# Kernel tuning notes

Measured on AMD Instinct MI355X. Metric: run time of the kernel, lower is better.

## Reference

```python
import jax, jax.numpy as jnp
import numpy as np

CLIP = 10.0  # tanh clipping constant (Kool et al. C=10)


def setup_inputs() -> dict:
    key = jax.random.key(0)
    kq, kk, kv, km = jax.random.split(key, 4)
    B, M, N, D = 16, 2048, 2048, 128
    Q = jax.random.normal(kq, (B, M, D), dtype=jnp.float32)
    K = jax.random.normal(kk, (B, N, D), dtype=jnp.float32)
    V = jax.random.normal(kv, (B, N, D), dtype=jnp.float32)
    # mask: [B, N, 1] bool; True means "forbidden" (set logit to -inf).
    # p=0.3 so every row keeps plenty of valid keys (no all-masked rows).
    mask = jax.random.bernoulli(km, 0.3, (B, N, 1))
    return {"Q": Q, "K": K, "V": V, "mask": mask}


def reference(Q, K, V, mask):
    d_k = jnp.asarray(K.shape[-1], dtype=Q.dtype)
    # logits: [B, M, N]
    logits = jnp.einsum("bmd,bnd->bmn", Q, K) / jnp.sqrt(d_k)
    logits = CLIP * jnp.tanh(logits)
    # mask [B, N, 1] -> [B, 1, N], broadcast over query dim
    mask_t = jnp.transpose(mask, (0, 2, 1))
    logits = jnp.where(mask_t, -jnp.inf, logits)
    probs = jax.nn.softmax(logits, axis=-1)
    return jnp.einsum("bmn,bnd->bmd", probs, V)
```

## Files before the change

### kernel.cpp

```cpp
#include <hip/hip_runtime.h>
#include <hip/hip_fp16.h>

typedef _Float16 h8 __attribute__((ext_vector_type(8)));
typedef _Float16 h4 __attribute__((ext_vector_type(4)));
typedef float f32x4 __attribute__((ext_vector_type(4)));
typedef float f32x16 __attribute__((ext_vector_type(16)));
typedef unsigned int u32x2 __attribute__((ext_vector_type(2)));
typedef unsigned int u32x4 __attribute__((ext_vector_type(4)));

#define MFMA16(a, b, c) __builtin_amdgcn_mfma_f32_16x16x32_f16((a), (b), (c), 0, 0, 0)
#define MFMA32(a, b, c) __builtin_amdgcn_mfma_f32_32x32x16_f16((a), (b), (c), 0, 0, 0)

static constexpr int MM = 2048, NN = 2048, DD = 128;
static constexpr int KT = 64, NT = NN / KT;
static constexpr size_t KV_IMG = (size_t)16 * 32 * 16384;
static constexpr size_t WS_NEED = 2 * KV_IMG + 4096 + 32768 * 4;

static constexpr float C1 = 0.25503487f;
static constexpr float C2 = 28.853900817779268f;
static constexpr float CVALID = 14.426950408889634f;
static constexpr float CMASK = -1.0e30f;

__device__ inline void glds16(const void* g, void* l) {
  __builtin_amdgcn_global_load_lds(
      (const __attribute__((address_space(1))) void*)g,
      (__attribute__((address_space(3))) void*)l, 16, 0, 0);
}

__global__ __launch_bounds__(256) void prep_bias(const void* __restrict__ mraw,
                                                 float* __restrict__ biasC) {
  const int tid = threadIdx.x;
  const unsigned int* mw = (const unsigned int*)mraw;
  const unsigned char* mby = (const unsigned char*)mraw;
  int okW = 1;
  for (int w = tid; w < 8192; w += 256) {
    unsigned int v = mw[w];
    okW &= (v == 0u || v == 1u || v == 0x3f800000u) ? 1 : 0;
  }
  __shared__ int sW;
  if (tid == 0) sW = 1;
  __syncthreads();
  if (!okW) atomicAnd(&sW, 0);
  __syncthreads();
  const int i = blockIdx.x * 256 + tid;
  bool masked = sW ? (mw[i] != 0u) : (mby[i] != 0);
  biasC[i] = masked ? CMASK : CVALID;
}

__global__ __launch_bounds__(256) void prep_all(
    const float* __restrict__ K, const float* __restrict__ V,
    const void* __restrict__ mraw, unsigned char* __restrict__ kimg,
    unsigned char* __restrict__ vimg, unsigned long long* __restrict__ m64) {
  const int id = blockIdx.x;
  const int tid = threadIdx.x;
  if (id >= 1024) {
    const unsigned int* mw = (const unsigned int*)mraw;
    const unsigned char* mby = (const unsigned char*)mraw;
    int okW = 1;
    for (int w = tid; w < 8192; w += 256) {
      unsigned int v = mw[w];
      okW &= (v == 0u || v == 1u || v == 0x3f800000u) ? 1 : 0;
    }
    __shared__ int sW;
    if (tid == 0) sW = 1;
    __syncthreads();
    if (!okW) atomicAnd(&sW, 0);
    __syncthreads();
    const int p = (id - 1024) * 256 + tid;
    const int base = p * 64;
    unsigned long long bits = 0ull;
    if (sW) {
#pragma unroll 8
      for (int k = 0; k < 64; ++k)
        bits |= (unsigned long long)(mw[base + k] != 0u ? 1 : 0) << k;
    } else {
#pragma unroll 8
      for (int k = 0; k < 64; ++k)
        bits |= (unsigned long long)(mby[base + k] != 0 ? 1 : 0) << k;
    }
    m64[p] = bits;
    return;
  }
  const int bt = id & 511;
  if (id < 512) {
    const float* src = K + (size_t)bt * KT * DD;
    unsigned char* dst = kimg + (size_t)bt * 16384;
#pragma unroll
    for (int it = 0; it < 4; ++it) {
      const int key = (tid >> 4) + 16 * it;
      const int o = tid & 15;
      f32x4 a = *(const f32x4*)(src + key * DD + 8 * o);
      f32x4 c = *(const f32x4*)(src + key * DD + 8 * o + 4);
      h8 hv;
#pragma unroll
      for (int j = 0; j < 4; ++j) {
        hv[j] = (_Float16)a[j];
        hv[j + 4] = (_Float16)c[j];
      }
      *(h8*)(dst + key * 256 + ((16 * o) ^ ((key & 7) << 4))) = hv;
    }
  } else {
    const float* src = V + (size_t)bt * KT * DD;
    unsigned char* dst = vimg + (size_t)bt * 16384;
    const int d = tid & 127;
    const int half = tid >> 7;
#pragma unroll
    for (int ki = 0; ki < 4; ++ki) {
      const int koct = half * 4 + ki;
      h8 w;
#pragma unroll
      for (int q = 0; q < 8; ++q)
        w[q] = (_Float16)src[(8 * koct + q) * DD + d];
      *(h8*)(dst + d * 128 + 16 * (koct ^ (d & 7))) = w;
    }
  }
}

__global__ __launch_bounds__(512, 2) void attn_main(
    const float* __restrict__ Qg, const unsigned char* __restrict__ kimg,
    const unsigned char* __restrict__ vimg,
    const unsigned long long* __restrict__ mask64, float* __restrict__ out) {
  __shared__ __align__(16) unsigned char smem[68096];
  const int tid = threadIdx.x;
  const int lane = tid & 63;
  const int wv = tid >> 6;
  const int l31 = lane & 31;
  const int hp = lane >> 5;
  const int qg = wv >> 1;
  const int h = wv & 1;
  const int bid = blockIdx.x;
  const int b = 2 * (bid & 7) + (bid >> 7);
  const int mt = (bid >> 3) & 15;
  const int m0 = mt * 128 + qg * 32;

  h8 qa[8];
  {
    const float* qr = Qg + ((size_t)b * MM + m0 + l31) * DD;
#pragma unroll
    for (int st = 0; st < 8; ++st) {
      const int d0 = 16 * st + 8 * hp;
      f32x4 a = *(const f32x4*)(qr + d0);
      f32x4 c = *(const f32x4*)(qr + d0 + 4);
      h8 hi;
#pragma unroll
      for (int j = 0; j < 4; ++j) {
        hi[j] = (_Float16)a[j];
        hi[j + 4] = (_Float16)c[j];
      }
      qa[st] = hi;
    }
  }

  f32x16 oacc[4];
#pragma unroll
  for (int dc = 0; dc < 4; ++dc)
#pragma unroll
    for (int j = 0; j < 16; ++j) oacc[dc][j] = 0.f;
  float rsl = 0.f;

  const unsigned char* kib = kimg + (size_t)b * 32 * 16384;
  const unsigned char* vib = vimg + (size_t)b * 32 * 16384;
  const unsigned long long* mtile = mask64 + (size_t)b * 32;

#pragma unroll
  for (int i = 0; i < 2; ++i) {
    const int off = wv * 2048 + i * 1024;
    glds16(kib + off + lane * 16, smem + off);
    glds16(vib + off + lane * 16, smem + 16384 + off);
  }
  __syncthreads();

  const int kr = 32 * h + l31;
  const int krow = kr << 8;
  const int ksw = (kr & 7) << 4;
  const int baseSh = 32 * h + 4 * hp;

  for (int tn = 0; tn < NT; ++tn) {
    const unsigned char* kbuf = smem + (tn & 1) * 32768;
    const unsigned char* vbuf = kbuf + 16384;
    if (tn + 1 < NT) {
      unsigned char* nbuf = smem + ((tn + 1) & 1) * 32768;
      const unsigned char* ks = kib + (size_t)(tn + 1) * 16384;
      const unsigned char* vs = vib + (size_t)(tn + 1) * 16384;
#pragma unroll
      for (int i = 0; i < 2; ++i) {
        const int off = wv * 2048 + i * 1024;
        glds16(ks + off + lane * 16, nbuf + off);
        glds16(vs + off + lane * 16, nbuf + 16384 + off);
      }
    }
    const unsigned long long mbits = mtile[tn];

    f32x16 s;
#pragma unroll
    for (int j = 0; j < 16; ++j) s[j] = 0.f;
    __builtin_amdgcn_s_setprio(1);
#pragma unroll
    for (int st = 0; st < 8; ++st) {
      h8 kf = *(const h8*)(kbuf + krow + ((32 * st + 16 * hp) ^ ksw));
      s = MFMA32(kf, qa[st], s);
    }
    __builtin_amdgcn_s_setprio(0);

    float p[16];
#pragma unroll
    for (int q = 0; q < 4; ++q) {
      const unsigned nib = (unsigned)(mbits >> (baseSh + 8 * q)) & 0xFu;
#pragma unroll
      for (int i = 0; i < 4; ++i) {
        const int rg = 4 * q + i;
        const float Cc = ((nib >> i) & 1u) ? CMASK : CVALID;
        const float u = __builtin_amdgcn_exp2f(s[rg] * C1);
        const float pv = __builtin_amdgcn_exp2f(
            fmaf(-C2, __builtin_amdgcn_rcpf(u + 1.0f), Cc));
        p[rg] = pv;
        rsl += pv;
      }
    }
    unsigned pkA[4], pkB[4];
#pragma unroll
    for (int q = 0; q < 4; ++q) {
      pkA[q] = __builtin_bit_cast(
          unsigned, __builtin_amdgcn_cvt_pkrtz(p[4 * q + 0], p[4 * q + 1]));
      pkB[q] = __builtin_bit_cast(
          unsigned, __builtin_amdgcn_cvt_pkrtz(p[4 * q + 2], p[4 * q + 3]));
    }
    h8 pb[2];
#pragma unroll
    for (int ks = 0; ks < 2; ++ks) {
      u32x2 sa = __builtin_amdgcn_permlane32_swap(pkA[2 * ks], pkA[2 * ks + 1],
                                                  false, false);
      u32x2 sb = __builtin_amdgcn_permlane32_swap(pkB[2 * ks], pkB[2 * ks + 1],
                                                  false, false);
      u32x4 w = {sa[0], sb[0], sa[1], sb[1]};
      pb[ks] = __builtin_bit_cast(h8, w);
    }
    __builtin_amdgcn_s_setprio(1);
#pragma unroll
    for (int dc = 0; dc < 4; ++dc) {
      const int d = 32 * dc + l31;
      const int vrow = d << 7;
      const int vsw = (d & 7) << 4;
      h8 vf0 = *(const h8*)(vbuf + vrow + ((64 * h + 16 * hp) ^ vsw));
      h8 vf1 = *(const h8*)(vbuf + vrow + ((64 * h + 32 + 16 * hp) ^ vsw));
      oacc[dc] = MFMA32(vf0, pb[0], oacc[dc]);
      oacc[dc] = MFMA32(vf1, pb[1], oacc[dc]);
    }
    __builtin_amdgcn_s_setprio(0);
    __syncthreads();
  }

  u32x2 rr = __builtin_amdgcn_permlane32_swap(__float_as_uint(rsl),
                                              __float_as_uint(rsl), false,
                                              false);
  const float totH = __uint_as_float(rr[0]) + __uint_as_float(rr[1]);

  float* olds = (float*)smem;
  float* rs1 = (float*)(smem + 67584);
  const int row = qg * 32 + l31;
  if (h == 1) {
#pragma unroll
    for (int dc = 0; dc < 4; ++dc)
#pragma unroll
      for (int q = 0; q < 4; ++q) {
        f32x4 v = {oacc[dc][4 * q + 0], oacc[dc][4 * q + 1],
                   oacc[dc][4 * q + 2], oacc[dc][4 * q + 3]};
        *(f32x4*)&olds[row * 132 + 32 * dc + 8 * q + 4 * hp] = v;
      }
    if (hp == 0) rs1[row] = totH;
  }
  __syncthreads();
  if (h == 0) {
    const float inv = __builtin_amdgcn_rcpf(totH + rs1[row]);
#pragma unroll
    for (int dc = 0; dc < 4; ++dc)
#pragma unroll
      for (int q = 0; q < 4; ++q) {
        float* pp = &olds[row * 132 + 32 * dc + 8 * q + 4 * hp];
        f32x4 v = *(const f32x4*)pp;
        v[0] = (v[0] + oacc[dc][4 * q + 0]) * inv;
        v[1] = (v[1] + oacc[dc][4 * q + 1]) * inv;
        v[2] = (v[2] + oacc[dc][4 * q + 2]) * inv;
        v[3] = (v[3] + oacc[dc][4 * q + 3]) * inv;
        *(f32x4*)pp = v;
      }
  }
  __syncthreads();
  float* ob = out + ((size_t)b * MM + mt * 128) * DD;
#pragma unroll
  for (int c = 0; c < 8; ++c) {
    const int idx = c * 2048 + tid * 4;
    const int r2 = idx >> 7, col = idx & 127;
    *(f32x4*)&ob[r2 * 128 + col] = *(const f32x4*)&olds[r2 * 132 + col];
  }
}

__global__ __launch_bounds__(256, 2) void attn_fallback(
    const float* __restrict__ Qg, const float* __restrict__ Kg,
    const float* __restrict__ Vg, const float* __restrict__ biasC,
    float* __restrict__ out) {
  __shared__ __align__(16) unsigned char smem[51456];
  const int tid = threadIdx.x;
  const int lane = tid & 63;
  const int wv = tid >> 6;
  const int r = lane & 15;
  const int g = lane >> 4;
  const int rw = wv >> 1;
  const int h = wv & 1;
  const int b = blockIdx.x >> 5;
  const int mt = blockIdx.x & 31;
  const int m0 = mt * 64 + rw * 32;

  float* blds = (float*)(smem + 43264);
  {
    const float* cb = biasC + b * NN;
#pragma unroll
    for (int i = 0; i < 8; ++i) blds[tid + 256 * i] = cb[tid + 256 * i];
  }
  h8 qh[2][4];
  {
    const float* qb = Qg + ((size_t)b * MM + m0) * DD;
#pragma unroll
    for (int rf = 0; rf < 2; ++rf) {
      const float* qr = qb + (16 * rf + r) * DD;
#pragma unroll
      for (int t = 0; t < 4; ++t) {
        f32x4 a = *(const f32x4*)(qr + 32 * t + 8 * g);
        f32x4 c = *(const f32x4*)(qr + 32 * t + 8 * g + 4);
        h8 hi;
#pragma unroll
        for (int j = 0; j < 4; ++j) {
          hi[j] = (_Float16)a[j];
          hi[j + 4] = (_Float16)c[j];
        }
        qh[rf][t] = hi;
      }
    }
  }
  f32x4 acc[2][8];
#pragma unroll
  for (int rf = 0; rf < 2; ++rf)
#pragma unroll
    for (int cd = 0; cd < 8; ++cd) acc[rf][cd] = (f32x4){0.f, 0.f, 0.f, 0.f};
  float rs[2][4] = {{0.f, 0.f, 0.f, 0.f}, {0.f, 0.f, 0.f, 0.f}};
  const float* kb = Kg + (size_t)b * NN * DD;
  const float* vbp = Vg + (size_t)b * NN * DD;
  _Float16* plds = (_Float16*)(smem + 32768 + wv * 2560);
  const int bk0 = tid >> 5, bd0 = tid & 31;
  const int bk1 = (256 + tid) >> 5, bd1 = tid & 31;
  f32x4 kpre[8], vpre[8];
#pragma unroll
  for (int i = 0; i < 8; ++i) kpre[i] = *(const f32x4*)(kb + i * 1024 + tid * 4);
#pragma unroll
  for (int q = 0; q < 4; ++q) {
    vpre[q] = *(const f32x4*)(vbp + (4 * bk0 + q) * DD + 4 * bd0);
    vpre[4 + q] = *(const f32x4*)(vbp + (4 * bk1 + q) * DD + 4 * bd1);
  }
  for (int tn = 0; tn < NT; ++tn) {
#pragma unroll
    for (int i = 0; i < 8; ++i) {
      const int flat = i * 1024 + tid * 4;
      const int kkey = flat >> 7;
      const int d0 = flat & 127;
      h4 hv;
#pragma unroll
      for (int j = 0; j < 4; ++j) hv[j] = (_Float16)kpre[i][j];
      *(h4*)(smem + (kkey << 8) + ((d0 << 1) ^ ((kkey & 7) << 4))) = hv;
    }
#pragma unroll
    for (int it = 0; it < 2; ++it) {
      const int bk = it ? bk1 : bk0;
      const int bd = it ? bd1 : bd0;
#pragma unroll
      for (int p = 0; p < 4; ++p) {
        h4 w;
#pragma unroll
        for (int q = 0; q < 4; ++q) w[q] = (_Float16)vpre[it * 4 + q][p];
        const int d = 4 * bd + p;
        *(h4*)(smem + 16384 + (d << 7) +
               ((bk << 3) ^ (((d >> 1) & 7) << 4))) = w;
      }
    }
    if (tn + 1 < NT) {
      const float* ks = kb + (tn + 1) * KT * DD;
      const float* vs = vbp + (tn + 1) * KT * DD;
#pragma unroll
      for (int i = 0; i < 8; ++i) kpre[i] = *(const f32x4*)(ks + i * 1024 + tid * 4);
#pragma unroll
      for (int q = 0; q < 4; ++q) {
        vpre[q] = *(const f32x4*)(vs + (4 * bk0 + q) * DD + 4 * bd0);
        vpre[4 + q] = *(const f32x4*)(vs + (4 * bk1 + q) * DD + 4 * bd1);
      }
    }
    __syncthreads();
#pragma unroll
    for (int c = 0; c < 2; ++c) {
      f32x4 S0 = {0.f, 0.f, 0.f, 0.f}, S1 = {0.f, 0.f, 0.f, 0.f};
      const int kkey = h * 32 + 16 * c + r;
      const int krow = kkey << 8;
      const int ksw = (kkey & 7) << 4;
#pragma unroll
      for (int t = 0; t < 4; ++t) {
        h8 kf = *(const h8*)(smem + krow + ((64 * t + 16 * g) ^ ksw));
        S0 = MFMA16(qh[0][t], kf, S0);
        S1 = MFMA16(qh[1][t], kf, S1);
      }
      const float Cc = blds[tn * KT + kkey];
#pragma unroll
      for (int j = 0; j < 4; ++j) {
        float u0 = __builtin_amdgcn_exp2f(S0[j] * C1);
        float p0 = __builtin_amdgcn_exp2f(
            fmaf(-C2, __builtin_amdgcn_rcpf(u0 + 1.0f), Cc));
        rs[0][j] += p0;
        plds[(4 * g + j) * 40 + 16 * c + r] = (_Float16)p0;
        float u1 = __builtin_amdgcn_exp2f(S1[j] * C1);
        float p1 = __builtin_amdgcn_exp2f(
            fmaf(-C2, __builtin_amdgcn_rcpf(u1 + 1.0f), Cc));
        rs[1][j] += p1;
        plds[(16 + 4 * g + j) * 40 + 16 * c + r] = (_Float16)p1;
      }
    }
    h8 a0 = *(const h8*)((unsigned char*)plds + r * 80 + 16 * g);
    h8 a1 = *(const h8*)((unsigned char*)plds + (16 + r) * 80 + 16 * g);
#pragma unroll
    for (int cd = 0; cd < 8; ++cd) {
      const int d = 16 * cd + r;
      h8 vf = *(const h8*)(smem + 16384 + (d << 7) +
                           ((64 * h + 16 * g) ^ (((d >> 1) & 7) << 4)));
      acc[0][cd] = MFMA16(a0, vf, acc[0][cd]);
      acc[1][cd] = MFMA16(a1, vf, acc[1][cd]);
    }
    __syncthreads();
  }
#pragma unroll
  for (int rf = 0; rf < 2; ++rf)
#pragma unroll
    for (int j = 0; j < 4; ++j) {
      float v = rs[rf][j];
      v += __shfl_xor(v, 1);
      v += __shfl_xor(v, 2);
      v += __shfl_xor(v, 4);
      v += __shfl_xor(v, 8);
      rs[rf][j] = v;
    }
  float* olds = (float*)smem;
  float* rslds = (float*)(smem + 43008);
  if (h == 1) {
    float* my = olds + rw * 4096;
#pragma unroll
    for (int rf = 0; rf < 2; ++rf)
#pragma unroll
      for (int cd = 0; cd < 8; ++cd)
#pragma unroll
        for (int j = 0; j < 4; ++j)
          my[(16 * rf + 4 * g + j) * 128 + 16 * cd + r] = acc[rf][cd][j];
    if (r == 0) {
#pragma unroll
      for (int rf = 0; rf < 2; ++rf)
#pragma unroll
        for (int j = 0; j < 4; ++j)
          rslds[rw * 32 + 16 * rf + 4 * g + j] = rs[rf][j];
    }
  }
  __syncthreads();
  if (h == 0) {
    const float* ot = olds + rw * 4096;
    float* ob = out + ((size_t)b * MM + m0) * DD;
#pragma unroll
    for (int rf = 0; rf < 2; ++rf)
#pragma unroll
      for (int j = 0; j < 4; ++j) {
        const int rl = 16 * rf + 4 * g + j;
        const float tot = rs[rf][j] + rslds[rw * 32 + rl];
        const float inv = __builtin_amdgcn_rcpf(tot);
#pragma unroll
        for (int cd = 0; cd < 8; ++cd) {
          float v = acc[rf][cd][j] + ot[rl * 128 + 16 * cd + r];
          ob[rl * DD + 16 * cd + r] = v * inv;
        }
      }
  }
}

extern "C" void kernel_launch(void* const* d_in, const int* in_sizes, int n_in,
                              void* d_out, int out_size, void* d_ws, size_t ws_size,
                              hipStream_t stream) {
  const float* Q = (const float*)d_in[0];
  const float* K = (const float*)d_in[1];
  const float* V = (const float*)d_in[2];
  const void* mask = d_in[3];
  float* out = (float*)d_out;
  if (ws_size >= WS_NEED) {
    unsigned char* kimg = (unsigned char*)d_ws;
    unsigned char* vimg = kimg + KV_IMG;
    unsigned long long* m64 = (unsigned long long*)(vimg + KV_IMG);
    prep_all<<<dim3(1026), dim3(256), 0, stream>>>(K, V, mask, kimg, vimg, m64);
    attn_main<<<dim3(256), dim3(512), 0, stream>>>(Q, kimg, vimg, m64, out);
  } else {
    float* biasC = (float*)d_ws;
    prep_bias<<<dim3(128), dim3(256), 0, stream>>>(mask, biasC);
    attn_fallback<<<dim3(512), dim3(256), 0, stream>>>(Q, K, V, biasC, out);
  }
}
```

Before: 82.02 us.

## Fold mask into V and row-sum MFMA, enlarge key tile to 128

Masking moves out of the softmax loop. Masked V rows are zeroed during preprocessing, and the row sum is computed by an MFMA against a per-key fp16 indicator vector, so the per-element mask select and scalar accumulation go away. The K image is pre-scaled by C1 to drop a multiply per logit. The key tile doubles to 128 with larger double-buffered LDS (about 135KB), which lowers occupancy to one block per CU in exchange for fewer barriers per key. Mask preprocessing becomes its own kernel launch, adding a dependency ahead of prep_kv.

Result: faster. 75.18 us (-8.3%).

```diff
diff --git a/kernel.cpp b/kernel.cpp
--- a/kernel.cpp
+++ b/kernel.cpp
@@ -12,9 +12,10 @@
 #define MFMA32(a, b, c) __builtin_amdgcn_mfma_f32_32x32x16_f16((a), (b), (c), 0, 0, 0)
 
 static constexpr int MM = 2048, NN = 2048, DD = 128;
-static constexpr int KT = 64, NT = NN / KT;
-static constexpr size_t KV_IMG = (size_t)16 * 32 * 16384;
-static constexpr size_t WS_NEED = 2 * KV_IMG + 4096 + 32768 * 4;
+static constexpr int KT = 128, NT = NN / KT;
+static constexpr size_t KV_IMG = (size_t)16 * 16 * 32768;
+static constexpr size_t IND_IMG = 65536;
+static constexpr size_t WS_NEED = 2 * KV_IMG + IND_IMG + 32768 * 4;
 
 static constexpr float C1 = 0.25503487f;
 static constexpr float C2 = 28.853900817779268f;
@@ -25,6 +26,26 @@
   __builtin_amdgcn_global_load_lds(
       (const __attribute__((address_space(1))) void*)g,
       (__attribute__((address_space(3))) void*)l, 16, 0, 0);
+}
+
+__global__ __launch_bounds__(256) void prep_mask(const void* __restrict__ mraw,
+                                                 _Float16* __restrict__ ind) {
+  const int tid = threadIdx.x;
+  const unsigned int* mw = (const unsigned int*)mraw;
+  const unsigned char* mby = (const unsigned char*)mraw;
+  int okW = 1;
+  for (int w = tid; w < 8192; w += 256) {
+    unsigned int v = mw[w];
+    okW &= (v == 0u || v == 1u || v == 0x3f800000u) ? 1 : 0;
+  }
+  __shared__ int sW;
+  if (tid == 0) sW = 1;
+  __syncthreads();
+  if (!okW) atomicAnd(&sW, 0);
+  __syncthreads();
+  const int i = blockIdx.x * 256 + tid;
+  bool masked = sW ? (mw[i] != 0u) : (mby[i] != 0);
+  ind[i] = masked ? (_Float16)0.0f : (_Float16)1.0f;
 }
 
 __global__ __launch_bounds__(256) void prep_bias(const void* __restrict__ mraw,
@@ -47,44 +68,17 @@
   biasC[i] = masked ? CMASK : CVALID;
 }
 
-__global__ __launch_bounds__(256) void prep_all(
-    const float* __restrict__ K, const float* __restrict__ V,
-    const void* __restrict__ mraw, unsigned char* __restrict__ kimg,
-    unsigned char* __restrict__ vimg, unsigned long long* __restrict__ m64) {
+__global__ __launch_bounds__(256) void prep_kv(const float* __restrict__ K,
+                                               const float* __restrict__ V,
+                                               const _Float16* __restrict__ ind,
+                                               unsigned char* __restrict__ kimg,
+                                               unsigned char* __restrict__ vimg) {
   const int id = blockIdx.x;
   const int tid = threadIdx.x;
-  if (id >= 1024) {
-    const unsigned int* mw = (const unsigned int*)mraw;
-    const unsigned char* mby = (const unsigned char*)mraw;
-    int okW = 1;
-    for (int w = tid; w < 8192; w += 256) {
-      unsigned int v = mw[w];
-      okW &= (v == 0u || v == 1u || v == 0x3f800000u) ? 1 : 0;
-    }
-    __shared__ int sW;
-    if (tid == 0) sW = 1;
-    __syncthreads();
-    if (!okW) atomicAnd(&sW, 0);
-    __syncthreads();
-    const int p = (id - 1024) * 256 + tid;
-    const int base = p * 64;
-    unsigned long long bits = 0ull;
-    if (sW) {
-#pragma unroll 8
-      for (int k = 0; k < 64; ++k)
-        bits |= (unsigned long long)(mw[base + k] != 0u ? 1 : 0) << k;
-    } else {
-#pragma unroll 8
-      for (int k = 0; k < 64; ++k)
-        bits |= (unsigned long long)(mby[base + k] != 0 ? 1 : 0) << k;
-    }
-    m64[p] = bits;
-    return;
-  }
-  const int bt = id & 511;
+  const int bt = (id < 512) ? id : (id - 512);
   if (id < 512) {
-    const float* src = K + (size_t)bt * KT * DD;
-    unsigned char* dst = kimg + (size_t)bt * 16384;
+    const float* src = K + (size_t)bt * 64 * DD;
+    unsigned char* dst = kimg + (size_t)(bt >> 1) * 32768 + (bt & 1) * 16384;
 #pragma unroll
     for (int it = 0; it < 4; ++it) {
       const int key = (tid >> 4) + 16 * it;
@@ -94,14 +88,15 @@
       h8 hv;
 #pragma unroll
       for (int j = 0; j < 4; ++j) {
-        hv[j] = (_Float16)a[j];
-        hv[j + 4] = (_Float16)c[j];
+        hv[j] = (_Float16)(a[j] * C1);
+        hv[j + 4] = (_Float16)(c[j] * C1);
       }
       *(h8*)(dst + key * 256 + ((16 * o) ^ ((key & 7) << 4))) = hv;
     }
   } else {
-    const float* src = V + (size_t)bt * KT * DD;
-    unsigned char* dst = vimg + (size_t)bt * 16384;
+    const float* src = V + (size_t)bt * 64 * DD;
+    unsigned char* dst = vimg + (size_t)(bt >> 1) * 32768;
+    const _Float16* ip = ind + (size_t)bt * 64;
     const int d = tid & 127;
     const int half = tid >> 7;
 #pragma unroll
@@ -110,17 +105,18 @@
       h8 w;
 #pragma unroll
       for (int q = 0; q < 8; ++q)
-        w[q] = (_Float16)src[(8 * koct + q) * DD + d];
-      *(h8*)(dst + d * 128 + 16 * (koct ^ (d & 7))) = w;
-    }
-  }
-}
-
-__global__ __launch_bounds__(512, 2) void attn_main(
+        w[q] = (_Float16)src[(8 * koct + q) * DD + d] * ip[8 * koct + q];
+      const int g = (bt & 1) * 8 + koct;
+      *(h8*)(dst + d * 256 + ((g * 16) ^ ((d & 7) << 4))) = w;
+    }
+  }
+}
+
+__global__ __launch_bounds__(512, 1) void attn_main(
     const float* __restrict__ Qg, const unsigned char* __restrict__ kimg,
-    const unsigned char* __restrict__ vimg,
-    const unsigned long long* __restrict__ mask64, float* __restrict__ out) {
-  __shared__ __align__(16) unsigned char smem[68096];
+    const unsigned char* __restrict__ vimg, const _Float16* __restrict__ indg,
+    float* __restrict__ out) {
+  __shared__ __align__(16) unsigned char smem[135680];
   const int tid = threadIdx.x;
   const int lane = tid & 63;
   const int wv = tid >> 6;
@@ -156,116 +152,121 @@
   for (int dc = 0; dc < 4; ++dc)
 #pragma unroll
     for (int j = 0; j < 16; ++j) oacc[dc][j] = 0.f;
-  float rsl = 0.f;
-
-  const unsigned char* kib = kimg + (size_t)b * 32 * 16384;
-  const unsigned char* vib = vimg + (size_t)b * 32 * 16384;
-  const unsigned long long* mtile = mask64 + (size_t)b * 32;
-
-#pragma unroll
-  for (int i = 0; i < 2; ++i) {
-    const int off = wv * 2048 + i * 1024;
+  f32x16 rsacc;
+#pragma unroll
+  for (int j = 0; j < 16; ++j) rsacc[j] = 0.f;
+
+  const unsigned char* kib = kimg + (size_t)b * 16 * 32768;
+  const unsigned char* vib = vimg + (size_t)b * 16 * 32768;
+  unsigned char* sind = smem + 131072;
+
+#pragma unroll
+  for (int i = 0; i < 4; ++i) {
+    const int off = wv * 4096 + i * 1024;
     glds16(kib + off + lane * 16, smem + off);
-    glds16(vib + off + lane * 16, smem + 16384 + off);
-  }
-  __syncthreads();
-
-  const int kr = 32 * h + l31;
-  const int krow = kr << 8;
-  const int ksw = (kr & 7) << 4;
-  const int baseSh = 32 * h + 4 * hp;
+    glds16(vib + off + lane * 16, smem + 32768 + off);
+  }
+  if (wv < 4)
+    glds16((const unsigned char*)indg + (size_t)b * 4096 + wv * 1024 + lane * 16,
+           sind + wv * 1024);
+  __syncthreads();
+
+  const int ksw = (l31 & 7) << 4;
 
   for (int tn = 0; tn < NT; ++tn) {
-    const unsigned char* kbuf = smem + (tn & 1) * 32768;
-    const unsigned char* vbuf = kbuf + 16384;
+    const unsigned char* kbuf = smem + (tn & 1) * 65536;
+    const unsigned char* vbuf = kbuf + 32768;
     if (tn + 1 < NT) {
-      unsigned char* nbuf = smem + ((tn + 1) & 1) * 32768;
-      const unsigned char* ks = kib + (size_t)(tn + 1) * 16384;
-      const unsigned char* vs = vib + (size_t)(tn + 1) * 16384;
-#pragma unroll
-      for (int i = 0; i < 2; ++i) {
-        const int off = wv * 2048 + i * 1024;
+      unsigned char* nbuf = smem + ((tn + 1) & 1) * 65536;
+      const unsigned char* ks = kib + (size_t)(tn + 1) * 32768;
+      const unsigned char* vs = vib + (size_t)(tn + 1) * 32768;
+#pragma unroll
+      for (int i = 0; i < 4; ++i) {
+        const int off = wv * 4096 + i * 1024;
         glds16(ks + off + lane * 16, nbuf + off);
-        glds16(vs + off + lane * 16, nbuf + 16384 + off);
-      }
-    }
-    const unsigned long long mbits = mtile[tn];
-
-    f32x16 s;
-#pragma unroll
-    for (int j = 0; j < 16; ++j) s[j] = 0.f;
-    __builtin_amdgcn_s_setprio(1);
-#pragma unroll
-    for (int st = 0; st < 8; ++st) {
-      h8 kf = *(const h8*)(kbuf + krow + ((32 * st + 16 * hp) ^ ksw));
-      s = MFMA32(kf, qa[st], s);
-    }
-    __builtin_amdgcn_s_setprio(0);
-
-    float p[16];
-#pragma unroll
-    for (int q = 0; q < 4; ++q) {
-      const unsigned nib = (unsigned)(mbits >> (baseSh + 8 * q)) & 0xFu;
-#pragma unroll
-      for (int i = 0; i < 4; ++i) {
-        const int rg = 4 * q + i;
-        const float Cc = ((nib >> i) & 1u) ? CMASK : CVALID;
-        const float u = __builtin_amdgcn_exp2f(s[rg] * C1);
-        const float pv = __builtin_amdgcn_exp2f(
-            fmaf(-C2, __builtin_amdgcn_rcpf(u + 1.0f), Cc));
-        p[rg] = pv;
-        rsl += pv;
-      }
-    }
-    unsigned pkA[4], pkB[4];
-#pragma unroll
-    for (int q = 0; q < 4; ++q) {
-      pkA[q] = __builtin_bit_cast(
-          unsigned, __builtin_amdgcn_cvt_pkrtz(p[4 * q + 0], p[4 * q + 1]));
-      pkB[q] = __builtin_bit_cast(
-          unsigned, __builtin_amdgcn_cvt_pkrtz(p[4 * q + 2], p[4 * q + 3]));
-    }
-    h8 pb[2];
-#pragma unroll
-    for (int ks = 0; ks < 2; ++ks) {
-      u32x2 sa = __builtin_amdgcn_permlane32_swap(pkA[2 * ks], pkA[2 * ks + 1],
-                                                  false, false);
-      u32x2 sb = __builtin_amdgcn_permlane32_swap(pkB[2 * ks], pkB[2 * ks + 1],
-                                                  false, false);
-      u32x4 w = {sa[0], sb[0], sa[1], sb[1]};
-      pb[ks] = __builtin_bit_cast(h8, w);
-    }
-    __builtin_amdgcn_s_setprio(1);
-#pragma unroll
-    for (int dc = 0; dc < 4; ++dc) {
-      const int d = 32 * dc + l31;
-      const int vrow = d << 7;
-      const int vsw = (d & 7) << 4;
-      h8 vf0 = *(const h8*)(vbuf + vrow + ((64 * h + 16 * hp) ^ vsw));
-      h8 vf1 = *(const h8*)(vbuf + vrow + ((64 * h + 32 + 16 * hp) ^ vsw));
-      oacc[dc] = MFMA32(vf0, pb[0], oacc[dc]);
-      oacc[dc] = MFMA32(vf1, pb[1], oacc[dc]);
-    }
-    __builtin_amdgcn_s_setprio(0);
+        glds16(vs + off + lane * 16, nbuf + 32768 + off);
+      }
+    }
+
+#pragma unroll
+    for (int c = 0; c < 2; ++c) {
+      f32x16 s;
+#pragma unroll
+      for (int j = 0; j < 16; ++j) s[j] = 0.f;
+      const int krow = (64 * h + 32 * c + l31) << 8;
+      __builtin_amdgcn_s_setprio(1);
+#pragma unroll
+      for (int st = 0; st < 8; ++st) {
+        h8 kf = *(const h8*)(kbuf + krow + ((32 * st + 16 * hp) ^ ksw));
+        s = MFMA32(kf, qa[st], s);
+      }
+      __builtin_amdgcn_s_setprio(0);
+
+      unsigned pkA[4], pkB[4];
+#pragma unroll
+      for (int jq = 0; jq < 4; ++jq) {
+        float p[4];
+#pragma unroll
+        for (int i = 0; i < 4; ++i) {
+          const float u = __builtin_amdgcn_exp2f(s[4 * jq + i]);
+          p[i] = __builtin_amdgcn_exp2f(
+              fmaf(-C2, __builtin_amdgcn_rcpf(u + 1.0f), CVALID));
+        }
+        pkA[jq] = __builtin_bit_cast(unsigned,
+                                     __builtin_amdgcn_cvt_pkrtz(p[0], p[1]));
+        pkB[jq] = __builtin_bit_cast(unsigned,
+                                     __builtin_amdgcn_cvt_pkrtz(p[2], p[3]));
+      }
+      h8 pb[2];
+#pragma unroll
+      for (int ks = 0; ks < 2; ++ks) {
+        u32x2 sa = __builtin_amdgcn_permlane32_swap(pkA[2 * ks],
+                                                    pkA[2 * ks + 1], false,
+                                                    false);
+        u32x2 sb = __builtin_amdgcn_permlane32_swap(pkB[2 * ks],
+                                                    pkB[2 * ks + 1], false,
+                                                    false);
+        u32x4 w = {sa[0], sb[0], sa[1], sb[1]};
+        pb[ks] = __builtin_bit_cast(h8, w);
+      }
+
+      __builtin_amdgcn_s_setprio(1);
+#pragma unroll
+      for (int ks = 0; ks < 2; ++ks) {
+        const int gks = 2 * c + ks;
+        h8 ia = *(const h8*)(sind + tn * 256 + 128 * h + 32 * gks + 16 * hp);
+        rsacc = MFMA32(ia, pb[ks], rsacc);
+      }
+#pragma unroll
+      for (int dc = 0; dc < 4; ++dc) {
+        const int vrow = (32 * dc + l31) << 8;
+#pragma unroll
+        for (int ks = 0; ks < 2; ++ks) {
+          const int gks = 2 * c + ks;
+          h8 vf = *(const h8*)(vbuf + vrow +
+                               ((128 * h + 32 * gks + 16 * hp) ^ ksw));
+          oacc[dc] = MFMA32(vf, pb[ks], oacc[dc]);
+        }
+      }
+      __builtin_amdgcn_s_setprio(0);
+    }
     __syncthreads();
   }
 
-  u32x2 rr = __builtin_amdgcn_permlane32_swap(__float_as_uint(rsl),
-                                              __float_as_uint(rsl), false,
-                                              false);
-  const float totH = __uint_as_float(rr[0]) + __uint_as_float(rr[1]);
-
-  float* olds = (float*)smem;
-  float* rs1 = (float*)(smem + 67584);
+  const float totH = rsacc[0];
+
+  float* rs1 = (float*)(smem + 135168);
+  unsigned char* olds = smem;
   const int row = qg * 32 + l31;
   if (h == 1) {
 #pragma unroll
     for (int dc = 0; dc < 4; ++dc)
 #pragma unroll
-      for (int q = 0; q < 4; ++q) {
-        f32x4 v = {oacc[dc][4 * q + 0], oacc[dc][4 * q + 1],
-                   oacc[dc][4 * q + 2], oacc[dc][4 * q + 3]};
-        *(f32x4*)&olds[row * 132 + 32 * dc + 8 * q + 4 * hp] = v;
+      for (int jq = 0; jq < 4; ++jq) {
+        f32x4 v = {oacc[dc][4 * jq + 0], oacc[dc][4 * jq + 1],
+                   oacc[dc][4 * jq + 2], oacc[dc][4 * jq + 3]};
+        const int dbyte = (32 * dc + 8 * jq + 4 * hp) * 4;
+        *(f32x4*)(olds + row * 512 + (dbyte ^ ((row & 31) << 4))) = v;
       }
     if (hp == 0) rs1[row] = totH;
   }
@@ -275,23 +276,26 @@
 #pragma unroll
     for (int dc = 0; dc < 4; ++dc)
 #pragma unroll
-      for (int q = 0; q < 4; ++q) {
-        float* pp = &olds[row * 132 + 32 * dc + 8 * q + 4 * hp];
+      for (int jq = 0; jq < 4; ++jq) {
+        const int dbyte = (32 * dc + 8 * jq + 4 * hp) * 4;
+        float* pp = (float*)(olds + row * 512 + (dbyte ^ ((row & 31) << 4)));
         f32x4 v = *(const f32x4*)pp;
-        v[0] = (v[0] + oacc[dc][4 * q + 0]) * inv;
-        v[1] = (v[1] + oacc[dc][4 * q + 1]) * inv;
-        v[2] = (v[2] + oacc[dc][4 * q + 2]) * inv;
-        v[3] = (v[3] + oacc[dc][4 * q + 3]) * inv;
+        v[0] = (v[0] + oacc[dc][4 * jq + 0]) * inv;
+        v[1] = (v[1] + oacc[dc][4 * jq + 1]) * inv;
+        v[2] = (v[2] + oacc[dc][4 * jq + 2]) * inv;
+        v[3] = (v[3] + oacc[dc][4 * jq + 3]) * inv;
         *(f32x4*)pp = v;
       }
   }
   __syncthreads();
   float* ob = out + ((size_t)b * MM + mt * 128) * DD;
 #pragma unroll
-  for (int c = 0; c < 8; ++c) {
-    const int idx = c * 2048 + tid * 4;
-    const int r2 = idx >> 7, col = idx & 127;
-    *(f32x4*)&ob[r2 * 128 + col] = *(const f32x4*)&olds[r2 * 132 + col];
+  for (int it = 0; it < 8; ++it) {
+    const int byte = it * 8192 + tid * 16;
+    const int r2 = byte >> 9;
+    const int g16 = byte & 511;
+    *(f32x4*)((unsigned char*)ob + byte) =
+        *(const f32x4*)(olds + r2 * 512 + (g16 ^ ((r2 & 31) << 4)));
   }
 }
 
@@ -356,7 +360,7 @@
     vpre[q] = *(const f32x4*)(vbp + (4 * bk0 + q) * DD + 4 * bd0);
     vpre[4 + q] = *(const f32x4*)(vbp + (4 * bk1 + q) * DD + 4 * bd1);
   }
-  for (int tn = 0; tn < NT; ++tn) {
+  for (int tn = 0; tn < 32; ++tn) {
 #pragma unroll
     for (int i = 0; i < 8; ++i) {
       const int flat = i * 1024 + tid * 4;
@@ -381,9 +385,9 @@
                ((bk << 3) ^ (((d >> 1) & 7) << 4))) = w;
       }
     }
-    if (tn + 1 < NT) {
-      const float* ks = kb + (tn + 1) * KT * DD;
-      const float* vs = vbp + (tn + 1) * KT * DD;
+    if (tn + 1 < 32) {
+      const float* ks = kb + (tn + 1) * 64 * DD;
+      const float* vs = vbp + (tn + 1) * 64 * DD;
 #pragma unroll
       for (int i = 0; i < 8; ++i) kpre[i] = *(const f32x4*)(ks + i * 1024 + tid * 4);
 #pragma unroll
@@ -405,7 +409,7 @@
         S0 = MFMA16(qh[0][t], kf, S0);
         S1 = MFMA16(qh[1][t], kf, S1);
       }
-      const float Cc = blds[tn * KT + kkey];
+      const float Cc = blds[tn * 64 + kkey];
 #pragma unroll
       for (int j = 0; j < 4; ++j) {
         float u0 = __builtin_amdgcn_exp2f(S0[j] * C1);
@@ -493,9 +497,10 @@
   if (ws_size >= WS_NEED) {
     unsigned char* kimg = (unsigned char*)d_ws;
     unsigned char* vimg = kimg + KV_IMG;
-    unsigned long long* m64 = (unsigned long long*)(vimg + KV_IMG);
-    prep_all<<<dim3(1026), dim3(256), 0, stream>>>(K, V, mask, kimg, vimg, m64);
-    attn_main<<<dim3(256), dim3(512), 0, stream>>>(Q, kimg, vimg, m64, out);
+    _Float16* ind = (_Float16*)(vimg + KV_IMG);
+    prep_mask<<<dim3(128), dim3(256), 0, stream>>>(mask, ind);
+    prep_kv<<<dim3(1024), dim3(256), 0, stream>>>(K, V, ind, kimg, vimg);
+    attn_main<<<dim3(256), dim3(512), 0, stream>>>(Q, kimg, vimg, ind, out);
   } else {
     float* biasC = (float*)d_ws;
     prep_bias<<<dim3(128), dim3(256), 0, stream>>>(mask, biasC);
```
